# Optimization experiments

Hardware: AMD Instinct MI355X
Metric: run time of the kernel (lower is better)

Reference implementation:

```python
import jax, jax.numpy as jnp
import numpy as np

N, D, H, O, E = 4096, 1024, 4096, 1024, 8
TOP_K = 2

def setup_inputs() -> dict:
    key = jax.random.key(0)
    k = jax.random.split(key, 4)
    x  = jax.random.normal(k[0], (N, D), dtype=jnp.float32)
    Wg = jax.random.normal(k[1], (D, E), dtype=jnp.float32) * (1.0 / np.sqrt(D))
    W1 = jax.random.normal(k[2], (E, D, H), dtype=jnp.float32) * (1.0 / np.sqrt(D))
    b1 = jnp.zeros((E, H), dtype=jnp.float32)
    W2 = jax.random.normal(k[3], (E, H, O), dtype=jnp.float32) * (1.0 / np.sqrt(H))
    b2 = jnp.zeros((E, O), dtype=jnp.float32)
    return {"x": x, "Wg": Wg, "W1": W1, "b1": b1, "W2": W2, "b2": b2}

def reference(x, Wg, W1, b1, W2, b2):
    # Gate: Linear(bias=False) -> ReLU (lin() appends act) -> softmax
    logits = jax.nn.relu(x @ Wg)                      # [N, E]
    probs = jax.nn.softmax(logits, axis=1)            # [N, E]
    top_p, sel = jax.lax.top_k(probs, TOP_K)          # [N, K]
    top_p = top_p / jnp.sum(top_p, axis=-1, keepdims=True)
    # Per-token combine weights over experts: [N, E]
    combine = jnp.sum(jax.nn.one_hot(sel, E, dtype=x.dtype) * top_p[..., None], axis=1)
    # Experts: ReLU(x W1 + b1) -> ReLU(h W2 + b2); final ReLU because lin() adds act on output layer
    h = jax.nn.relu(jnp.einsum('nd,edh->enh', x, W1) + b1[:, None, :])   # [E, N, H]
    y = jax.nn.relu(jnp.einsum('enh,eho->eno', h, W2) + b2[:, None, :])  # [E, N, O]
    out = jnp.einsum('eno,ne->no', y, combine)                            # [N, O]
    return out
```

## Files before the change

kernel.cpp:

```cpp
#include <hip/hip_runtime.h>
#include <cstdint>

#define NTOK 4096
#define DDIM 1024
#define HDIM 4096
#define ODIM 1024
#define NEXP 8
#define NSLOT (2*NTOK)
#define MAXT128 72

typedef __bf16 bf16x8 __attribute__((ext_vector_type(8)));
typedef float  f32x4  __attribute__((ext_vector_type(4)));
typedef unsigned short ushort8v __attribute__((ext_vector_type(8)));

__device__ __forceinline__ unsigned short f2bf(float f) {
    union { float f; unsigned int u; } v; v.f = f;
    unsigned int r = (v.u + 0x7FFF + ((v.u >> 16) & 1)) >> 16;
    return (unsigned short)r;
}

typedef const void __attribute__((address_space(1)))* gas_ptr;
typedef void       __attribute__((address_space(3)))* las_ptr;

template <int N> __device__ __forceinline__ void vm_wait() {
    if constexpr (N == 0) asm volatile("s_waitcnt vmcnt(0)" ::: "memory");
    else if constexpr (N == 3) asm volatile("s_waitcnt vmcnt(3)" ::: "memory");
    else if constexpr (N == 4) asm volatile("s_waitcnt vmcnt(4)" ::: "memory");
    else if constexpr (N == 6) asm volatile("s_waitcnt vmcnt(6)" ::: "memory");
}

__global__ void gate_kernel(const float* __restrict__ x, const float* __restrict__ Wg,
                            int2* __restrict__ sel, float2* __restrict__ wts,
                            int* __restrict__ counts, unsigned short* __restrict__ xb) {
    int wave = threadIdx.x >> 6;
    int lane = threadIdx.x & 63;
    int n = blockIdx.x * 4 + wave;
    float acc[NEXP];
#pragma unroll
    for (int e = 0; e < NEXP; e++) acc[e] = 0.f;
    const float* xr = x + (size_t)n * DDIM;
    unsigned short* xbr = xb + (size_t)n * DDIM;
#pragma unroll
    for (int i = 0; i < 4; i++) {
        int d = i * 256 + lane * 4;
        float4 xv = *(const float4*)&xr[d];
        ushort4 o;
        o.x = f2bf(xv.x); o.y = f2bf(xv.y); o.z = f2bf(xv.z); o.w = f2bf(xv.w);
        *(ushort4*)&xbr[d] = o;
        const float* wr = Wg + (size_t)d * NEXP;
#pragma unroll
        for (int jj = 0; jj < 4; jj++) {
            float xs = (jj == 0) ? xv.x : (jj == 1) ? xv.y : (jj == 2) ? xv.z : xv.w;
#pragma unroll
            for (int e = 0; e < NEXP; e++)
                acc[e] = fmaf(xs, wr[jj * NEXP + e], acc[e]);
        }
    }
#pragma unroll
    for (int e = 0; e < NEXP; e++) {
#pragma unroll
        for (int off = 32; off >= 1; off >>= 1)
            acc[e] += __shfl_xor(acc[e], off, 64);
    }
    if (lane == 0) {
        float l0 = -1e30f, l1 = -1e30f; int e0 = 0, e1 = 0;
#pragma unroll
        for (int e = 0; e < NEXP; e++) {
            float v = fmaxf(acc[e], 0.f);
            if (v > l0)      { l1 = l0; e1 = e0; l0 = v; e0 = e; }
            else if (v > l1) { l1 = v;  e1 = e; }
        }
        float w0 = 1.f / (1.f + expf(l1 - l0));
        sel[n] = make_int2(e0, e1);
        wts[n] = make_float2(w0, 1.f - w0);
        atomicAdd(&counts[e0], 1);
        atomicAdd(&counts[e1], 1);
    }
}

__global__ void route_kernel(const int2* __restrict__ sel, const float2* __restrict__ wts,
                             const int* __restrict__ counts, int* __restrict__ offsets,
                             int4* __restrict__ t128, int* __restrict__ nt128,
                             int* __restrict__ slot_token, float* __restrict__ slot_weight,
                             int2* __restrict__ tokslot) {
    __shared__ int cur[NEXP];
    int t = threadIdx.x;
    if (t == 0) {
        int s = 0, n1 = 0;
        for (int e = 0; e < NEXP; e++) {
            offsets[e] = s; cur[e] = s;
            int c = counts[e];
            for (int r = 0; r < c; r += 128)
                t128[n1++] = make_int4(e, s + r, min(128, c - r), 0);
            s += c;
        }
        offsets[NEXP] = s;
        *nt128 = n1;
    }
    __syncthreads();
    for (int n = t; n < NTOK; n += blockDim.x) {
        int2 se = sel[n]; float2 w = wts[n];
        int p0 = atomicAdd(&cur[se.x], 1);
        slot_token[p0] = n; slot_weight[p0] = w.x;
        int p1 = atomicAdd(&cur[se.y], 1);
        slot_token[p1] = n; slot_weight[p1] = w.y;
        tokslot[n] = make_int2(p0, p1);
    }
}

__global__ void transpose_cast_kernel(const float* __restrict__ src, unsigned short* __restrict__ dst,
                                      int R, int C) {
    __shared__ float tile[64][65];
    int e = blockIdx.z;
    const float* s = src + (size_t)e * R * C;
    unsigned short* d = dst + (size_t)e * R * C;
    int t = threadIdx.x;
    int r0 = blockIdx.y * 64, c0 = blockIdx.x * 64;
#pragma unroll
    for (int p = 0; p < 4; p++) {
        int r = p * 16 + (t >> 4);
        int c = (t & 15) * 4;
        float4 v = *(const float4*)&s[(size_t)(r0 + r) * C + (c0 + c)];
        tile[r][c] = v.x; tile[r][c + 1] = v.y; tile[r][c + 2] = v.z; tile[r][c + 3] = v.w;
    }
    __syncthreads();
    int c = t >> 2, rb = (t & 3) * 16;
#pragma unroll
    for (int j = 0; j < 2; j++) {
        ushort8v v;
#pragma unroll
        for (int i = 0; i < 8; i++) v[i] = f2bf(tile[rb + j * 8 + i][c]);
        *(ushort8v*)&d[(size_t)(c0 + c) * R + (r0 + rb + j * 8)] = v;
    }
}

template <int MODE, int KDIM, int NDIM, int THREADS, int TN, int WM, int WN, int MINW, int NCOL>
__global__ __launch_bounds__(THREADS, MINW) void moe_gemm_kernel(
    const unsigned short* __restrict__ A,
    const unsigned short* __restrict__ B,
    const float* __restrict__ bias,
    const int4* __restrict__ tile_meta,
    const int* __restrict__ ntiles,
    const int* __restrict__ slot_token,
    unsigned short* __restrict__ h,
    float* __restrict__ yout) {

    constexpr int TM = 128;
    constexpr int RM = TM / WM, RN = TN / WN;
    constexpr int FM = RM / 16, FN = RN / 16;
    constexpr int NT = KDIM / 32;
    constexpr int LA = TM * 4 / THREADS;
    constexpr int LB = TN * 4 / THREADS;
    constexpr int L  = LA + LB;

    constexpr int nwg = NCOL * MAXT128;
    int bid = blockIdx.y * NCOL + blockIdx.x;
    int o = (bid & 7) * (nwg >> 3) + (bid >> 3);
    int tg = o / (8 * NCOL);
    int rem = o - tg * (8 * NCOL);
    int col = rem >> 3;
    int tile = tg * 8 + (rem & 7);
    if (tile >= *ntiles) return;
    int colBase = col * TN;

    int4 tm = tile_meta[tile];
    int e = tm.x, slotBase = tm.y, rows = tm.z;

    __shared__ __align__(16) unsigned short As[3][TM * 32];
    __shared__ __align__(16) unsigned short Bs[3][TN * 32];

    int tid = threadIdx.x;
    int w = tid >> 6, lane = tid & 63;
    int quad = lane >> 4, lr = lane & 15;
    int wm = w / WN, wn = w % WN;

    const unsigned short* Be = B + (size_t)e * NDIM * KDIM;

    unsigned int aoff[LA];
    unsigned int boff[LB];
#pragma unroll
    for (int i = 0; i < LA; i++) {
        int u = i * THREADS + tid;
        int r = u >> 2, g = (u & 3) ^ ((u >> 3) & 3);
        int slot = min(slotBase + r, NSLOT - 1);
        if constexpr (MODE == 1) aoff[i] = (unsigned)(slot_token[slot] * KDIM + g * 8);
        else                     aoff[i] = (unsigned)(slot * KDIM + g * 8);
    }
#pragma unroll
    for (int i = 0; i < LB; i++) {
        int u = i * THREADS + tid;
        int r = u >> 2, g = (u & 3) ^ ((u >> 3) & 3);
        boff[i] = (unsigned)((colBase + r) * KDIM + g * 8);
    }

    auto stage = [&](int t, int sbuf) {
        char* Ab = (char*)&As[sbuf][0] + w * 1024;
        char* Bb = (char*)&Bs[sbuf][0] + w * 1024;
#pragma unroll
        for (int i = 0; i < LA; i++)
            __builtin_amdgcn_global_load_lds((gas_ptr)(A + aoff[i] + t * 32),
                                             (las_ptr)(Ab + i * THREADS * 16), 16, 0, 0);
#pragma unroll
        for (int i = 0; i < LB; i++)
            __builtin_amdgcn_global_load_lds((gas_ptr)(Be + boff[i] + t * 32),
                                             (las_ptr)(Bb + i * THREADS * 16), 16, 0, 0);
    };

    auto rdfrags = [&](bf16x8 (&af)[FM], bf16x8 (&bf)[FN], int buf) {
        const char* Ar = (const char*)&As[buf][0];
        const char* Br = (const char*)&Bs[buf][0];
#pragma unroll
        for (int m = 0; m < FM; m++) {
            int R = wm * RM + m * 16 + lr;
            int s = quad ^ ((R >> 1) & 3);
            af[m] = *(const bf16x8*)(Ar + R * 64 + s * 16);
        }
#pragma unroll
        for (int n = 0; n < FN; n++) {
            int R = wn * RN + n * 16 + lr;
            int s = quad ^ ((R >> 1) & 3);
            bf[n] = *(const bf16x8*)(Br + R * 64 + s * 16);
        }
    };

    f32x4 zero = {0.f, 0.f, 0.f, 0.f};
    f32x4 acc[FM][FN];
#pragma unroll
    for (int m = 0; m < FM; m++)
#pragma unroll
        for (int n = 0; n < FN; n++) acc[m][n] = zero;

    auto mfma_all = [&](bf16x8 (&af)[FM], bf16x8 (&bf)[FN]) {
        __builtin_amdgcn_s_setprio(1);
#pragma unroll
        for (int m = 0; m < FM; m++)
#pragma unroll
            for (int n = 0; n < FN; n++)
                acc[m][n] = __builtin_amdgcn_mfma_f32_16x16x32_bf16(bf[n], af[m], acc[m][n], 0, 0, 0);
        __builtin_amdgcn_s_setprio(0);
    };

    bf16x8 afA[FM], bfA[FN], afB[FM], bfB[FN];

    stage(0, 0);
    stage(1, 1);
    vm_wait<L>();
    __builtin_amdgcn_s_barrier();
    rdfrags(afA, bfA, 0);
    asm volatile("s_waitcnt lgkmcnt(0)" ::: "memory");
    __builtin_amdgcn_sched_barrier(0);

    int sb = 2, rb = 1;
    for (int t = 0; t < NT; t += 2) {
        bool st2 = (t + 2 < NT);
        if (st2) stage(t + 2, sb);
        if (st2) vm_wait<L>(); else vm_wait<0>();
        __builtin_amdgcn_s_barrier();
        rdfrags(afB, bfB, rb);
        mfma_all(afA, bfA);
        asm volatile("s_waitcnt lgkmcnt(0)" ::: "memory");
        __builtin_amdgcn_sched_barrier(0);
        __builtin_amdgcn_s_barrier();
        sb = (sb == 2) ? 0 : sb + 1;
        rb = (rb == 2) ? 0 : rb + 1;

        bool st3 = (t + 3 < NT);
        if (st3) stage(t + 3, sb);
        if (st2) { if (st3) vm_wait<L>(); else vm_wait<0>(); }
        __builtin_amdgcn_s_barrier();
        if (st2) rdfrags(afA, bfA, rb);
        mfma_all(afB, bfB);
        asm volatile("s_waitcnt lgkmcnt(0)" ::: "memory");
        __builtin_amdgcn_sched_barrier(0);
        __builtin_amdgcn_s_barrier();
        sb = (sb == 2) ? 0 : sb + 1;
        rb = (rb == 2) ? 0 : rb + 1;
    }

    const float* bv = bias + e * NDIM;
    if constexpr (MODE == 1) {
#pragma unroll
        for (int m = 0; m < FM; m++) {
            int r = wm * RM + m * 16 + lr;
            if (r < rows) {
                unsigned short* hrow = h + (size_t)(slotBase + r) * NDIM;
#pragma unroll
                for (int n = 0; n < FN; n++) {
                    int c = colBase + wn * RN + n * 16 + quad * 4;
                    float4 bb = *(const float4*)&bv[c];
                    unsigned int lo = (unsigned)f2bf(fmaxf(acc[m][n][0] + bb.x, 0.f)) |
                                      ((unsigned)f2bf(fmaxf(acc[m][n][1] + bb.y, 0.f)) << 16);
                    unsigned int hi = (unsigned)f2bf(fmaxf(acc[m][n][2] + bb.z, 0.f)) |
                                      ((unsigned)f2bf(fmaxf(acc[m][n][3] + bb.w, 0.f)) << 16);
                    uint2 pv = make_uint2(lo, hi);
                    *(uint2*)&hrow[c] = pv;
                }
            }
        }
    } else {
#pragma unroll
        for (int m = 0; m < FM; m++) {
            int r = wm * RM + m * 16 + lr;
            if (r < rows) {
                float* yrow = yout + (size_t)(slotBase + r) * NDIM;
#pragma unroll
                for (int n = 0; n < FN; n++) {
                    int c = colBase + wn * RN + n * 16 + quad * 4;
                    float4 bb = *(const float4*)&bv[c];
                    float4 v;
                    v.x = fmaxf(acc[m][n][0] + bb.x, 0.f);
                    v.y = fmaxf(acc[m][n][1] + bb.y, 0.f);
                    v.z = fmaxf(acc[m][n][2] + bb.z, 0.f);
                    v.w = fmaxf(acc[m][n][3] + bb.w, 0.f);
                    *(float4*)&yrow[c] = v;
                }
            }
        }
    }
}

__global__ void combine_kernel(const float* __restrict__ y, const int2* __restrict__ tokslot,
                               const float2* __restrict__ wts, float* __restrict__ out) {
    int n = blockIdx.x;
    int t = threadIdx.x;
    int2 ts = tokslot[n];
    float2 w = wts[n];
    float4 a = *(const float4*)&y[(size_t)ts.x * ODIM + t * 4];
    float4 b = *(const float4*)&y[(size_t)ts.y * ODIM + t * 4];
    float4 o;
    o.x = w.x * a.x + w.y * b.x;
    o.y = w.x * a.y + w.y * b.y;
    o.z = w.x * a.z + w.y * b.z;
    o.w = w.x * a.w + w.y * b.w;
    *(float4*)&out[(size_t)n * ODIM + t * 4] = o;
}

extern "C" void kernel_launch(void* const* d_in, const int* in_sizes, int n_in,
                              void* d_out, int out_size, void* d_ws, size_t ws_size,
                              hipStream_t stream) {
    const float* x  = (const float*)d_in[0];
    const float* Wg = (const float*)d_in[1];
    const float* W1 = (const float*)d_in[2];
    const float* b1 = (const float*)d_in[3];
    const float* W2 = (const float*)d_in[4];
    const float* b2 = (const float*)d_in[5];
    float* out = (float*)d_out;

    char* ws = (char*)d_ws;
    int*    counts      = (int*)(ws + 0);
    int*    offsets     = (int*)(ws + 64);
    int*    nt128       = (int*)(ws + 128);
    int4*   t128        = (int4*)(ws + 256);
    int2*   sel         = (int2*)(ws + 4096);
    float2* wts         = (float2*)(ws + 36864);
    int*    slot_token  = (int*)(ws + 69632);
    float*  slot_weight = (float*)(ws + 102400);
    int2*   tokslot     = (int2*)(ws + 135168);
    unsigned short* xb  = (unsigned short*)(ws + 2097152);
    unsigned short* W1T = (unsigned short*)(ws + 10485760);
    unsigned short* W2T = (unsigned short*)(ws + 77594624);
    unsigned short* hbf = (unsigned short*)(ws + 144703488);
    float* ybf = (float*)(ws + 10485760);

    hipMemsetAsync(ws, 0, 256, stream);

    gate_kernel<<<NTOK / 4, 256, 0, stream>>>(x, Wg, sel, wts, counts, xb);
    route_kernel<<<1, 512, 0, stream>>>(sel, wts, counts, offsets, t128, nt128,
                                        slot_token, slot_weight, tokslot);

    transpose_cast_kernel<<<dim3(HDIM / 64, DDIM / 64, NEXP), 256, 0, stream>>>(W1, W1T, DDIM, HDIM);
    transpose_cast_kernel<<<dim3(ODIM / 64, HDIM / 64, NEXP), 256, 0, stream>>>(W2, W2T, HDIM, ODIM);

    moe_gemm_kernel<1, DDIM, HDIM, 512, 256, 2, 4, 2, 16><<<dim3(16, MAXT128), 512, 0, stream>>>(
        xb, W1T, b1, t128, nt128, slot_token, hbf, nullptr);
    moe_gemm_kernel<2, HDIM, ODIM, 256, 128, 2, 2, 2, 8><<<dim3(8, MAXT128), 256, 0, stream>>>(
        hbf, W2T, b2, t128, nt128, slot_token, nullptr, ybf);

    combine_kernel<<<NTOK, 256, 0, stream>>>(ybf, tokslot, wts, out);
}
```

Baseline: 715.7 us.

## Replace LDS-staged MoE GEMM with direct global-to-register fragment loads

Replaces the triple-buffered shared-memory pipeline (global_load_lds, swizzled LDS reads, barriers) with a kernel where each wave loads its MFMA operand fragments straight from global memory into registers, double-buffered across k-steps. The first GEMM moves to 128x128 tiles with 256 threads instead of 128x256 with 512. This removes LDS traffic and block-wide barriers. In exchange it loses the cross-wave data sharing that LDS gave, so global and L2 traffic rise, and the per-lane loads of 16 bytes at row stride may coalesce poorly.

```diff
diff --git a/kernel.cpp b/kernel.cpp
--- a/kernel.cpp
+++ b/kernel.cpp
@@ -17,16 +17,6 @@
     union { float f; unsigned int u; } v; v.f = f;
     unsigned int r = (v.u + 0x7FFF + ((v.u >> 16) & 1)) >> 16;
     return (unsigned short)r;
-}
-
-typedef const void __attribute__((address_space(1)))* gas_ptr;
-typedef void       __attribute__((address_space(3)))* las_ptr;
-
-template <int N> __device__ __forceinline__ void vm_wait() {
-    if constexpr (N == 0) asm volatile("s_waitcnt vmcnt(0)" ::: "memory");
-    else if constexpr (N == 3) asm volatile("s_waitcnt vmcnt(3)" ::: "memory");
-    else if constexpr (N == 4) asm volatile("s_waitcnt vmcnt(4)" ::: "memory");
-    else if constexpr (N == 6) asm volatile("s_waitcnt vmcnt(6)" ::: "memory");
 }
 
 __global__ void gate_kernel(const float* __restrict__ x, const float* __restrict__ Wg,
@@ -134,8 +124,8 @@
     }
 }
 
-template <int MODE, int KDIM, int NDIM, int THREADS, int TN, int WM, int WN, int MINW, int NCOL>
-__global__ __launch_bounds__(THREADS, MINW) void moe_gemm_kernel(
+template <int MODE, int KDIM, int NDIM, int NCOL>
+__global__ __launch_bounds__(256, 2) void moe_gemm_direct(
     const unsigned short* __restrict__ A,
     const unsigned short* __restrict__ B,
     const float* __restrict__ bias,
@@ -145,13 +135,7 @@
     unsigned short* __restrict__ h,
     float* __restrict__ yout) {
 
-    constexpr int TM = 128;
-    constexpr int RM = TM / WM, RN = TN / WN;
-    constexpr int FM = RM / 16, FN = RN / 16;
-    constexpr int NT = KDIM / 32;
-    constexpr int LA = TM * 4 / THREADS;
-    constexpr int LB = TN * 4 / THREADS;
-    constexpr int L  = LA + LB;
+    constexpr int FM = 4, FN = 4;
 
     constexpr int nwg = NCOL * MAXT128;
     int bid = blockIdx.y * NCOL + blockIdx.x;
@@ -161,66 +145,39 @@
     int col = rem >> 3;
     int tile = tg * 8 + (rem & 7);
     if (tile >= *ntiles) return;
-    int colBase = col * TN;
+    int colBase = col * 128;
 
     int4 tm = tile_meta[tile];
     int e = tm.x, slotBase = tm.y, rows = tm.z;
-
-    __shared__ __align__(16) unsigned short As[3][TM * 32];
-    __shared__ __align__(16) unsigned short Bs[3][TN * 32];
 
     int tid = threadIdx.x;
     int w = tid >> 6, lane = tid & 63;
     int quad = lane >> 4, lr = lane & 15;
-    int wm = w / WN, wn = w % WN;
+    int wm = w >> 1, wn = w & 1;
 
     const unsigned short* Be = B + (size_t)e * NDIM * KDIM;
 
-    unsigned int aoff[LA];
-    unsigned int boff[LB];
-#pragma unroll
-    for (int i = 0; i < LA; i++) {
-        int u = i * THREADS + tid;
-        int r = u >> 2, g = (u & 3) ^ ((u >> 3) & 3);
+    unsigned int aoff[FM], boff[FN];
+#pragma unroll
+    for (int m = 0; m < FM; m++) {
+        int r = wm * 64 + m * 16 + lr;
         int slot = min(slotBase + r, NSLOT - 1);
-        if constexpr (MODE == 1) aoff[i] = (unsigned)(slot_token[slot] * KDIM + g * 8);
-        else                     aoff[i] = (unsigned)(slot * KDIM + g * 8);
-    }
-#pragma unroll
-    for (int i = 0; i < LB; i++) {
-        int u = i * THREADS + tid;
-        int r = u >> 2, g = (u & 3) ^ ((u >> 3) & 3);
-        boff[i] = (unsigned)((colBase + r) * KDIM + g * 8);
-    }
-
-    auto stage = [&](int t, int sbuf) {
-        char* Ab = (char*)&As[sbuf][0] + w * 1024;
-        char* Bb = (char*)&Bs[sbuf][0] + w * 1024;
-#pragma unroll
-        for (int i = 0; i < LA; i++)
-            __builtin_amdgcn_global_load_lds((gas_ptr)(A + aoff[i] + t * 32),
-                                             (las_ptr)(Ab + i * THREADS * 16), 16, 0, 0);
-#pragma unroll
-        for (int i = 0; i < LB; i++)
-            __builtin_amdgcn_global_load_lds((gas_ptr)(Be + boff[i] + t * 32),
-                                             (las_ptr)(Bb + i * THREADS * 16), 16, 0, 0);
-    };
-
-    auto rdfrags = [&](bf16x8 (&af)[FM], bf16x8 (&bf)[FN], int buf) {
-        const char* Ar = (const char*)&As[buf][0];
-        const char* Br = (const char*)&Bs[buf][0];
-#pragma unroll
-        for (int m = 0; m < FM; m++) {
-            int R = wm * RM + m * 16 + lr;
-            int s = quad ^ ((R >> 1) & 3);
-            af[m] = *(const bf16x8*)(Ar + R * 64 + s * 16);
-        }
-#pragma unroll
-        for (int n = 0; n < FN; n++) {
-            int R = wn * RN + n * 16 + lr;
-            int s = quad ^ ((R >> 1) & 3);
-            bf[n] = *(const bf16x8*)(Br + R * 64 + s * 16);
-        }
+        int arow;
+        if constexpr (MODE == 1) arow = slot_token[slot];
+        else                     arow = slot;
+        aoff[m] = (unsigned)(arow * KDIM + quad * 8);
+    }
+#pragma unroll
+    for (int n = 0; n < FN; n++) {
+        int r = colBase + wn * 64 + n * 16 + lr;
+        boff[n] = (unsigned)(r * KDIM + quad * 8);
+    }
+
+    auto ldset = [&](bf16x8 (&af)[FM], bf16x8 (&bf)[FN], int k) {
+#pragma unroll
+        for (int m = 0; m < FM; m++) af[m] = *(const bf16x8*)(A + aoff[m] + k);
+#pragma unroll
+        for (int n = 0; n < FN; n++) bf[n] = *(const bf16x8*)(Be + boff[n] + k);
     };
 
     f32x4 zero = {0.f, 0.f, 0.f, 0.f};
@@ -230,7 +187,7 @@
 #pragma unroll
         for (int n = 0; n < FN; n++) acc[m][n] = zero;
 
-    auto mfma_all = [&](bf16x8 (&af)[FM], bf16x8 (&bf)[FN]) {
+    auto domfma = [&](bf16x8 (&af)[FM], bf16x8 (&bf)[FN]) {
         __builtin_amdgcn_s_setprio(1);
 #pragma unroll
         for (int m = 0; m < FM; m++)
@@ -240,53 +197,25 @@
         __builtin_amdgcn_s_setprio(0);
     };
 
-    bf16x8 afA[FM], bfA[FN], afB[FM], bfB[FN];
-
-    stage(0, 0);
-    stage(1, 1);
-    vm_wait<L>();
-    __builtin_amdgcn_s_barrier();
-    rdfrags(afA, bfA, 0);
-    asm volatile("s_waitcnt lgkmcnt(0)" ::: "memory");
-    __builtin_amdgcn_sched_barrier(0);
-
-    int sb = 2, rb = 1;
-    for (int t = 0; t < NT; t += 2) {
-        bool st2 = (t + 2 < NT);
-        if (st2) stage(t + 2, sb);
-        if (st2) vm_wait<L>(); else vm_wait<0>();
-        __builtin_amdgcn_s_barrier();
-        rdfrags(afB, bfB, rb);
-        mfma_all(afA, bfA);
-        asm volatile("s_waitcnt lgkmcnt(0)" ::: "memory");
-        __builtin_amdgcn_sched_barrier(0);
-        __builtin_amdgcn_s_barrier();
-        sb = (sb == 2) ? 0 : sb + 1;
-        rb = (rb == 2) ? 0 : rb + 1;
-
-        bool st3 = (t + 3 < NT);
-        if (st3) stage(t + 3, sb);
-        if (st2) { if (st3) vm_wait<L>(); else vm_wait<0>(); }
-        __builtin_amdgcn_s_barrier();
-        if (st2) rdfrags(afA, bfA, rb);
-        mfma_all(afB, bfB);
-        asm volatile("s_waitcnt lgkmcnt(0)" ::: "memory");
-        __builtin_amdgcn_sched_barrier(0);
-        __builtin_amdgcn_s_barrier();
-        sb = (sb == 2) ? 0 : sb + 1;
-        rb = (rb == 2) ? 0 : rb + 1;
+    bf16x8 a0[FM], b0[FN], a1[FM], b1[FN];
+    ldset(a0, b0, 0);
+    for (int k = 0; k < KDIM; k += 64) {
+        ldset(a1, b1, k + 32);
+        domfma(a0, b0);
+        if (k + 64 < KDIM) ldset(a0, b0, k + 64);
+        domfma(a1, b1);
     }
 
     const float* bv = bias + e * NDIM;
     if constexpr (MODE == 1) {
 #pragma unroll
         for (int m = 0; m < FM; m++) {
-            int r = wm * RM + m * 16 + lr;
+            int r = wm * 64 + m * 16 + lr;
             if (r < rows) {
                 unsigned short* hrow = h + (size_t)(slotBase + r) * NDIM;
 #pragma unroll
                 for (int n = 0; n < FN; n++) {
-                    int c = colBase + wn * RN + n * 16 + quad * 4;
+                    int c = colBase + wn * 64 + n * 16 + quad * 4;
                     float4 bb = *(const float4*)&bv[c];
                     unsigned int lo = (unsigned)f2bf(fmaxf(acc[m][n][0] + bb.x, 0.f)) |
                                       ((unsigned)f2bf(fmaxf(acc[m][n][1] + bb.y, 0.f)) << 16);
@@ -300,12 +229,12 @@
     } else {
 #pragma unroll
         for (int m = 0; m < FM; m++) {
-            int r = wm * RM + m * 16 + lr;
+            int r = wm * 64 + m * 16 + lr;
             if (r < rows) {
                 float* yrow = yout + (size_t)(slotBase + r) * NDIM;
 #pragma unroll
                 for (int n = 0; n < FN; n++) {
-                    int c = colBase + wn * RN + n * 16 + quad * 4;
+                    int c = colBase + wn * 64 + n * 16 + quad * 4;
                     float4 bb = *(const float4*)&bv[c];
                     float4 v;
                     v.x = fmaxf(acc[m][n][0] + bb.x, 0.f);
@@ -371,9 +300,9 @@
     transpose_cast_kernel<<<dim3(HDIM / 64, DDIM / 64, NEXP), 256, 0, stream>>>(W1, W1T, DDIM, HDIM);
     transpose_cast_kernel<<<dim3(ODIM / 64, HDIM / 64, NEXP), 256, 0, stream>>>(W2, W2T, HDIM, ODIM);
 
-    moe_gemm_kernel<1, DDIM, HDIM, 512, 256, 2, 4, 2, 16><<<dim3(16, MAXT128), 512, 0, stream>>>(
+    moe_gemm_direct<1, DDIM, HDIM, 32><<<dim3(32, MAXT128), 256, 0, stream>>>(
         xb, W1T, b1, t128, nt128, slot_token, hbf, nullptr);
-    moe_gemm_kernel<2, HDIM, ODIM, 256, 128, 2, 2, 2, 8><<<dim3(8, MAXT128), 256, 0, stream>>>(
+    moe_gemm_direct<2, HDIM, ODIM, 8><<<dim3(8, MAXT128), 256, 0, stream>>>(
         hbf, W2T, b2, t128, nt128, slot_token, nullptr, ybf);
 
     combine_kernel<<<NTOK, 256, 0, stream>>>(ybf, tokslot, wts, out);
```

New measurement: 1.062 ms. +48.4%, slower.
